# Kernel tuning notes

Hardware: AMD Instinct MI355X
Metric: run time of the kernel (lower is better)

Reference implementation:

```python
import math
import jax, jax.numpy as jnp
import numpy as np

NA = 50000   # number of query nodes
NB = 50000   # number of key/value nodes
E = 800000   # number of edges
CA = 256
CB = 256
D = 256
H = 8
DH = D // H


def setup_inputs() -> dict:
    key = jax.random.key(0)
    ks = jax.random.split(key, 8)
    s = 1.0 / math.sqrt(CA)
    return {
        "Fa": jax.random.normal(ks[0], (NA, CA), dtype=jnp.float32),
        "Fb": jax.random.normal(ks[1], (NB, CB), dtype=jnp.float32),
        "a_idx": jax.random.randint(ks[2], (E,), 0, NA, dtype=jnp.int64)
        if jax.config.jax_enable_x64 else jax.random.randint(ks[2], (E,), 0, NA, dtype=jnp.int32),
        "b_idx": jax.random.randint(ks[3], (E,), 0, NB, dtype=jnp.int64)
        if jax.config.jax_enable_x64 else jax.random.randint(ks[3], (E,), 0, NB, dtype=jnp.int32),
        # torch nn.Linear weights: (out_features, in_features), y = x @ W.T
        "Wq": jax.random.normal(ks[4], (D, CA), dtype=jnp.float32) * s,
        "Wk": jax.random.normal(ks[5], (D, CB), dtype=jnp.float32) * s,
        "Wv": jax.random.normal(ks[6], (D, CB), dtype=jnp.float32) * s,
        "Wproj": jax.random.normal(ks[7], (CA, D), dtype=jnp.float32) * s,
    }


def _edge_attention(Q, K, V, Q_idx, K_idx, n_queries):
    # Q: (Na,H,dh)  K,V: (Nb,H,dh)  Q_idx,K_idx: (E,)
    scale = 1.0 / math.sqrt(Q.shape[-1])
    logits = jnp.sum(Q[Q_idx] * K[K_idx], axis=-1) * scale      # (E, H)
    # segmented softmax over edges sharing the same query (per head)
    seg_max = jax.ops.segment_max(logits, Q_idx, num_segments=n_queries)  # (Na, H)
    seg_max = jnp.where(jnp.isfinite(seg_max), seg_max, 0.0)
    ex = jnp.exp(logits - seg_max[Q_idx])                        # (E, H)
    seg_sum = jax.ops.segment_sum(ex, Q_idx, num_segments=n_queries)      # (Na, H)
    weights = ex / jnp.maximum(seg_sum[Q_idx], 1e-30)            # (E, H)
    # scatter-add weighted values
    out = jax.ops.segment_sum(weights[..., None] * V[K_idx], Q_idx,
                              num_segments=n_queries)            # (Na, H, dh)
    return out


def reference(Fa, Fb, a_idx, b_idx, Wq, Wk, Wv, Wproj):
    Na = Fa.shape[0]
    Q = (Fa @ Wq.T).reshape(Na, H, DH)
    K = (Fb @ Wk.T).reshape(-1, H, DH)
    V = (Fb @ Wv.T).reshape(-1, H, DH)
    out = _edge_attention(Q, K, V, a_idx, b_idx, Na)
    out = out.reshape(Na, H * DH)
    return Fa + out @ Wproj.T
```

## Files before the change

kernel.cpp:

```cpp
#include <hip/hip_runtime.h>

#define DM 256

typedef __attribute__((ext_vector_type(8))) short bf16x8;
typedef __attribute__((ext_vector_type(4))) float f32x4;
typedef __attribute__((ext_vector_type(4))) unsigned short us16x4;
typedef __attribute__((ext_vector_type(8))) unsigned short us16x8;
typedef unsigned short us16;

__device__ __forceinline__ unsigned short f2bf(float f) {
  unsigned int u = __float_as_uint(f);
  u += 0x7fffu + ((u >> 16) & 1u);
  return (unsigned short)(u >> 16);
}
__device__ __forceinline__ float bf2f(unsigned short s) {
  return __uint_as_float(((unsigned int)s) << 16);
}

__device__ __forceinline__ void gload16(const void* g, void* l) {
  __builtin_amdgcn_global_load_lds(
      (const __attribute__((address_space(1))) void*)g,
      (__attribute__((address_space(3))) void*)l, 16, 0, 0);
}

__global__ __launch_bounds__(512) void qkv_gemm(
    const float* __restrict__ Fa, const float* __restrict__ Fb,
    const us16* __restrict__ W_all, us16* __restrict__ Qbf,
    us16* __restrict__ KVbf, int NA, int NB)
{
  const int z = blockIdx.z;
  const float* A = (z == 0) ? Fa : Fb;
  const int Mreal = (z == 0) ? NA : NB;
  const int Mp = (Mreal + 127) & ~127;
  const us16* W = W_all + (size_t)z * 256 * 256;
  us16* Cb = (z == 0) ? Qbf : KVbf;
  const int ldc = (z == 0) ? 256 : 512;

  __shared__ us16 As[128 * 32];
  __shared__ us16 Bs[256 * 32];
  const int tid = threadIdx.x;
  const int w = tid >> 6, l = tid & 63;
  const int wr = w >> 2, wc = w & 3;
  const int rowBase = blockIdx.x * 128;
  if (rowBase >= Mp) return;
  const int ar = tid >> 2, ac = (tid & 3) * 8;
  f32x4 acc[4][4] = {};

  for (int k0 = 0; k0 < 256; k0 += 32) {
#pragma unroll
    for (int j = 0; j < 2; ++j) {
      const int r0 = (w * 2 + j) * 16;
      gload16(W + (size_t)(r0 + (l >> 2)) * 256 + k0 + (l & 3) * 8, &Bs[r0 * 32]);
    }
    {
      const int grow = rowBase + ar;
      bf16x8 av = (bf16x8){0, 0, 0, 0, 0, 0, 0, 0};
      if (grow < Mreal) {
        const float4 x = *(const float4*)(A + (size_t)grow * 256 + k0 + ac);
        const float4 y = *(const float4*)(A + (size_t)grow * 256 + k0 + ac + 4);
        av[0] = (short)f2bf(x.x); av[1] = (short)f2bf(x.y);
        av[2] = (short)f2bf(x.z); av[3] = (short)f2bf(x.w);
        av[4] = (short)f2bf(y.x); av[5] = (short)f2bf(y.y);
        av[6] = (short)f2bf(y.z); av[7] = (short)f2bf(y.w);
      }
      *(bf16x8*)&As[ar * 32 + ac] = av;
    }
    __syncthreads();
    bf16x8 af[4], bfr[4];
#pragma unroll
    for (int m = 0; m < 4; ++m)
      af[m] = *(const bf16x8*)&As[(wr * 64 + m * 16 + (l & 15)) * 32 + (l >> 4) * 8];
#pragma unroll
    for (int n = 0; n < 4; ++n)
      bfr[n] = *(const bf16x8*)&Bs[(wc * 64 + n * 16 + (l & 15)) * 32 + (l >> 4) * 8];
#pragma unroll
    for (int m = 0; m < 4; ++m)
#pragma unroll
      for (int n = 0; n < 4; ++n)
        acc[m][n] = __builtin_amdgcn_mfma_f32_16x16x32_bf16(af[m], bfr[n], acc[m][n], 0, 0, 0);
    __syncthreads();
  }

  const int er = (l >> 4) * 4;
  const int ec = l & 15;
  const int vofs = (z == 2) ? 4 : 0;
#pragma unroll
  for (int m = 0; m < 4; ++m)
#pragma unroll
    for (int n = 0; n < 4; ++n)
#pragma unroll
      for (int j = 0; j < 4; ++j) {
        const int grow = rowBase + wr * 64 + m * 16 + er + j;
        const int c = wc * 64 + n * 16 + ec;
        const int col = (z == 0) ? c : ((c >> 2) * 8 + (c & 3) + vofs);
        Cb[(size_t)grow * ldc + col] = f2bf(acc[m][n][j]);
      }
}

__global__ __launch_bounds__(512) void proj_gemm(
    const us16* __restrict__ A, const us16* __restrict__ W,
    float* __restrict__ Cf, const float* __restrict__ R, int Mreal)
{
  __shared__ us16 As[128 * 32];
  __shared__ us16 Bs[256 * 32];
  const int tid = threadIdx.x;
  const int w = tid >> 6, l = tid & 63;
  const int wr = w >> 2, wc = w & 3;
  const int rowBase = blockIdx.x * 128;
  const int ar = tid >> 2, ac = (tid & 3) * 8;
  f32x4 acc[4][4] = {};

  for (int k0 = 0; k0 < 256; k0 += 32) {
#pragma unroll
    for (int j = 0; j < 2; ++j) {
      const int r0 = (w * 2 + j) * 16;
      gload16(W + (size_t)(r0 + (l >> 2)) * 256 + k0 + (l & 3) * 8, &Bs[r0 * 32]);
    }
    *(bf16x8*)&As[ar * 32 + ac] =
        *(const bf16x8*)(A + (size_t)(rowBase + ar) * 256 + k0 + ac);
    __syncthreads();
    bf16x8 af[4], bfr[4];
#pragma unroll
    for (int m = 0; m < 4; ++m)
      af[m] = *(const bf16x8*)&As[(wr * 64 + m * 16 + (l & 15)) * 32 + (l >> 4) * 8];
#pragma unroll
    for (int n = 0; n < 4; ++n)
      bfr[n] = *(const bf16x8*)&Bs[(wc * 64 + n * 16 + (l & 15)) * 32 + (l >> 4) * 8];
#pragma unroll
    for (int m = 0; m < 4; ++m)
#pragma unroll
      for (int n = 0; n < 4; ++n)
        acc[m][n] = __builtin_amdgcn_mfma_f32_16x16x32_bf16(af[m], bfr[n], acc[m][n], 0, 0, 0);
    __syncthreads();
  }

  const int er = (l >> 4) * 4;
  const int ec = l & 15;
#pragma unroll
  for (int m = 0; m < 4; ++m)
#pragma unroll
    for (int n = 0; n < 4; ++n)
#pragma unroll
      for (int j = 0; j < 4; ++j) {
        const int grow = rowBase + wr * 64 + m * 16 + er + j;
        if (grow < Mreal) {
          const size_t off = (size_t)grow * 256 + wc * 64 + n * 16 + ec;
          Cf[off] = acc[m][n][j] + R[off];
        }
      }
}

__global__ void cvt_weights(const float* __restrict__ Wq, const float* __restrict__ Wk,
                            const float* __restrict__ Wv, const float* __restrict__ Wp,
                            us16* __restrict__ out)
{
  const int g = blockIdx.x * 256 + threadIdx.x;
  const size_t e = (size_t)g * 8;
  const int sel = (int)(e >> 16);
  const float* src = (sel == 0) ? Wq : (sel == 1) ? Wk : (sel == 2) ? Wv : Wp;
  const size_t loc = e & 65535;
  const float4 x = *(const float4*)(src + loc);
  const float4 y = *(const float4*)(src + loc + 4);
  bf16x8 o;
  o[0] = (short)f2bf(x.x); o[1] = (short)f2bf(x.y);
  o[2] = (short)f2bf(x.z); o[3] = (short)f2bf(x.w);
  o[4] = (short)f2bf(y.x); o[5] = (short)f2bf(y.y);
  o[6] = (short)f2bf(y.z); o[7] = (short)f2bf(y.w);
  *(bf16x8*)(out + e) = o;
}

__global__ void hist_kernel(const int* __restrict__ a_idx, int* __restrict__ counts, int E)
{
  const int e = blockIdx.x * 256 + threadIdx.x;
  if (e < E) atomicAdd(&counts[a_idx[e]], 1);
}

__global__ __launch_bounds__(256) void scan_offs(const int* __restrict__ counts,
    int* __restrict__ offs, int* __restrict__ cursor, int* __restrict__ total, int n)
{
  __shared__ int buf[256];
  __shared__ int sbase;
  const int t = threadIdx.x;
  const int i = blockIdx.x * 256 + t;
  const int v = (i < n) ? counts[i] : 0;
  buf[t] = v;
  __syncthreads();
#pragma unroll
  for (int off = 1; off < 256; off <<= 1) {
    const int x = (t >= off) ? buf[t - off] : 0;
    __syncthreads();
    buf[t] += x;
    __syncthreads();
  }
  const int incl = buf[t];
  if (t == 255) sbase = atomicAdd(total, incl);
  __syncthreads();
  if (i < n) {
    const int excl = sbase + incl - v;
    offs[i] = excl;
    cursor[i] = excl;
  }
}

__global__ void scatter_kernel(const int* __restrict__ a_idx, const int* __restrict__ b_idx,
    int* __restrict__ cursor, int* __restrict__ bel, int E)
{
  const int e = blockIdx.x * 256 + threadIdx.x;
  if (e < E) bel[atomicAdd(&cursor[a_idx[e]], 1)] = b_idx[e];
}

#define ATTN_STEP(S, J)                                        \
  if ((J) < cnt) {                                             \
    float p = q0 * bf2f(S[0]);                                 \
    p = fmaf(q1, bf2f(S[1]), p);                               \
    p = fmaf(q2, bf2f(S[2]), p);                               \
    p = fmaf(q3, bf2f(S[3]), p);                               \
    p += __shfl_xor(p, 1, 64);                                 \
    p += __shfl_xor(p, 2, 64);                                 \
    p += __shfl_xor(p, 4, 64);                                 \
    const float ex = __expf(p * scale);                        \
    ssum += ex;                                                \
    acc0 = fmaf(ex, bf2f(S[4]), acc0);                         \
    acc1 = fmaf(ex, bf2f(S[5]), acc1);                         \
    acc2 = fmaf(ex, bf2f(S[6]), acc2);                         \
    acc3 = fmaf(ex, bf2f(S[7]), acc3);                         \
  }

#define ATTN_LOAD(S, IDX)                                      \
  S = *(const us16x8*)(KVb + (size_t)bel[start + (IDX)] * 512 + l * 8);

__global__ __launch_bounds__(256) void edge_attn(
    const us16* __restrict__ Qb, const us16* __restrict__ KVb,
    const int* __restrict__ offs, const int* __restrict__ counts,
    const int* __restrict__ bel, us16* __restrict__ outb, int NA)
{
  const int a = blockIdx.x * 4 + (threadIdx.x >> 6);
  if (a >= NA) return;
  const int l = threadIdx.x & 63;
  const float scale = 0.17677669529663687f;

  const us16x4 q4 = *(const us16x4*)(Qb + (size_t)a * 256 + l * 4);
  const float q0 = bf2f(q4[0]), q1 = bf2f(q4[1]), q2 = bf2f(q4[2]), q3 = bf2f(q4[3]);

  const int start = offs[a];
  const int cnt = counts[a];
  float acc0 = 0.f, acc1 = 0.f, acc2 = 0.f, acc3 = 0.f, ssum = 0.f;

  if (cnt > 0) {
    const int last = cnt - 1;
    us16x8 sa, sb, sc, sd;
    ATTN_LOAD(sa, 0)
    ATTN_LOAD(sb, min(1, last))
    ATTN_LOAD(sc, min(2, last))
    ATTN_LOAD(sd, min(3, last))
    for (int i = 0; i < cnt; i += 4) {
      us16x8 na, nb, nc, nd;
      ATTN_LOAD(na, min(i + 4, last))
      ATTN_LOAD(nb, min(i + 5, last))
      ATTN_LOAD(nc, min(i + 6, last))
      ATTN_LOAD(nd, min(i + 7, last))
      ATTN_STEP(sa, i + 0)
      ATTN_STEP(sb, i + 1)
      ATTN_STEP(sc, i + 2)
      ATTN_STEP(sd, i + 3)
      sa = na; sb = nb; sc = nc; sd = nd;
    }
  }

  const float inv = (cnt > 0) ? 1.f / ssum : 0.f;
  us16x4 o;
  o[0] = f2bf(acc0 * inv); o[1] = f2bf(acc1 * inv);
  o[2] = f2bf(acc2 * inv); o[3] = f2bf(acc3 * inv);
  *(us16x4*)(outb + (size_t)a * 256 + l * 4) = o;
}

extern "C" void kernel_launch(void* const* d_in, const int* in_sizes, int n_in,
                              void* d_out, int out_size, void* d_ws, size_t ws_size,
                              hipStream_t stream)
{
  const float* Fa    = (const float*)d_in[0];
  const float* Fb    = (const float*)d_in[1];
  const int*   a_idx = (const int*)d_in[2];
  const int*   b_idx = (const int*)d_in[3];
  const float* Wq    = (const float*)d_in[4];
  const float* Wk    = (const float*)d_in[5];
  const float* Wv    = (const float*)d_in[6];
  const float* Wproj = (const float*)d_in[7];
  float* out = (float*)d_out;

  const int NA = in_sizes[0] / DM;
  const int NB = in_sizes[1] / DM;
  const int E  = in_sizes[2];
  const int MAp = (NA + 127) & ~127;
  const int NBp = (NB + 127) & ~127;
  const int MXp = (MAp > NBp) ? MAp : NBp;

  us16* Qbf   = (us16*)d_ws;
  us16* KVbf  = Qbf   + (size_t)MAp * 256;
  us16* ATbf  = KVbf  + (size_t)NBp * 512;
  us16* W_all = ATbf  + (size_t)MAp * 256;
  int* total  = (int*)(W_all + 1024 * 256);
  int* counts = total + 1;
  int* offs   = counts + NA;
  int* cursor = offs + NA;
  int* bel    = cursor + NA;

  hipMemsetAsync(total, 0, (size_t)(NA + 1) * sizeof(int), stream);

  cvt_weights<<<128, 256, 0, stream>>>(Wq, Wk, Wv, Wproj, W_all);

  hist_kernel<<<(E + 255) / 256, 256, 0, stream>>>(a_idx, counts, E);
  scan_offs<<<(NA + 255) / 256, 256, 0, stream>>>(counts, offs, cursor, total, NA);
  scatter_kernel<<<(E + 255) / 256, 256, 0, stream>>>(a_idx, b_idx, cursor, bel, E);

  qkv_gemm<<<dim3(MXp / 128, 1, 3), 512, 0, stream>>>(Fa, Fb, W_all, Qbf, KVbf, NA, NB);

  edge_attn<<<(NA + 3) / 4, 256, 0, stream>>>(Qbf, KVbf, offs, counts, bel, ATbf, NA);

  proj_gemm<<<dim3(MAp / 128, 1), 512, 0, stream>>>(ATbf, W_all + 768 * 256, out, Fa, NA);
}
```

Before: 448.3 us.

## Double-buffer LDS tiles in QKV and projection GEMMs to overlap loads with MFMA

Both GEMM kernels now use two LDS buffers for A and B tiles. The next K-slice is prefetched while MFMAs run on the current one, leaving one barrier per iteration instead of two. The projection GEMM also loads its A tile with global_load_lds direct-to-LDS instead of going through registers. This is meant to hide global load latency, at the cost of doubled shared memory (48KB per block), which may limit occupancy.

```diff
diff --git a/kernel.cpp b/kernel.cpp
--- a/kernel.cpp
+++ b/kernel.cpp
@@ -36,48 +36,71 @@
   us16* Cb = (z == 0) ? Qbf : KVbf;
   const int ldc = (z == 0) ? 256 : 512;
 
-  __shared__ us16 As[128 * 32];
-  __shared__ us16 Bs[256 * 32];
+  __shared__ us16 As[2][128 * 32];
+  __shared__ us16 Bs[2][256 * 32];
   const int tid = threadIdx.x;
   const int w = tid >> 6, l = tid & 63;
   const int wr = w >> 2, wc = w & 3;
   const int rowBase = blockIdx.x * 128;
   if (rowBase >= Mp) return;
   const int ar = tid >> 2, ac = (tid & 3) * 8;
+  const int grow0 = rowBase + ar;
+  const bool aval = grow0 < Mreal;
+  const float* Ap = A + (size_t)grow0 * 256 + ac;
   f32x4 acc[4][4] = {};
 
-  for (int k0 = 0; k0 < 256; k0 += 32) {
+  {
+    float4 x = make_float4(0.f, 0.f, 0.f, 0.f), y = x;
+    if (aval) { x = *(const float4*)(Ap); y = *(const float4*)(Ap + 4); }
 #pragma unroll
     for (int j = 0; j < 2; ++j) {
       const int r0 = (w * 2 + j) * 16;
-      gload16(W + (size_t)(r0 + (l >> 2)) * 256 + k0 + (l & 3) * 8, &Bs[r0 * 32]);
-    }
-    {
-      const int grow = rowBase + ar;
-      bf16x8 av = (bf16x8){0, 0, 0, 0, 0, 0, 0, 0};
-      if (grow < Mreal) {
-        const float4 x = *(const float4*)(A + (size_t)grow * 256 + k0 + ac);
-        const float4 y = *(const float4*)(A + (size_t)grow * 256 + k0 + ac + 4);
-        av[0] = (short)f2bf(x.x); av[1] = (short)f2bf(x.y);
-        av[2] = (short)f2bf(x.z); av[3] = (short)f2bf(x.w);
-        av[4] = (short)f2bf(y.x); av[5] = (short)f2bf(y.y);
-        av[6] = (short)f2bf(y.z); av[7] = (short)f2bf(y.w);
+      gload16(W + (size_t)(r0 + (l >> 2)) * 256 + (l & 3) * 8, &Bs[0][r0 * 32]);
+    }
+    bf16x8 av;
+    av[0] = (short)f2bf(x.x); av[1] = (short)f2bf(x.y);
+    av[2] = (short)f2bf(x.z); av[3] = (short)f2bf(x.w);
+    av[4] = (short)f2bf(y.x); av[5] = (short)f2bf(y.y);
+    av[6] = (short)f2bf(y.z); av[7] = (short)f2bf(y.w);
+    *(bf16x8*)&As[0][ar * 32 + ac] = av;
+  }
+  __syncthreads();
+
+  for (int t = 0; t < 8; ++t) {
+    const int cur = t & 1, nxt = cur ^ 1;
+    const bool pf = (t < 7);
+    float4 x, y;
+    if (pf) {
+      const int k0 = (t + 1) * 32;
+      x = make_float4(0.f, 0.f, 0.f, 0.f); y = x;
+      if (aval) { x = *(const float4*)(Ap + k0); y = *(const float4*)(Ap + k0 + 4); }
+#pragma unroll
+      for (int j = 0; j < 2; ++j) {
+        const int r0 = (w * 2 + j) * 16;
+        gload16(W + (size_t)(r0 + (l >> 2)) * 256 + k0 + (l & 3) * 8,
+                &Bs[nxt][r0 * 32]);
       }
-      *(bf16x8*)&As[ar * 32 + ac] = av;
-    }
-    __syncthreads();
+    }
     bf16x8 af[4], bfr[4];
 #pragma unroll
     for (int m = 0; m < 4; ++m)
-      af[m] = *(const bf16x8*)&As[(wr * 64 + m * 16 + (l & 15)) * 32 + (l >> 4) * 8];
+      af[m] = *(const bf16x8*)&As[cur][(wr * 64 + m * 16 + (l & 15)) * 32 + (l >> 4) * 8];
 #pragma unroll
     for (int n = 0; n < 4; ++n)
-      bfr[n] = *(const bf16x8*)&Bs[(wc * 64 + n * 16 + (l & 15)) * 32 + (l >> 4) * 8];
+      bfr[n] = *(const bf16x8*)&Bs[cur][(wc * 64 + n * 16 + (l & 15)) * 32 + (l >> 4) * 8];
 #pragma unroll
     for (int m = 0; m < 4; ++m)
 #pragma unroll
       for (int n = 0; n < 4; ++n)
         acc[m][n] = __builtin_amdgcn_mfma_f32_16x16x32_bf16(af[m], bfr[n], acc[m][n], 0, 0, 0);
+    if (pf) {
+      bf16x8 av;
+      av[0] = (short)f2bf(x.x); av[1] = (short)f2bf(x.y);
+      av[2] = (short)f2bf(x.z); av[3] = (short)f2bf(x.w);
+      av[4] = (short)f2bf(y.x); av[5] = (short)f2bf(y.y);
+      av[6] = (short)f2bf(y.z); av[7] = (short)f2bf(y.w);
+      *(bf16x8*)&As[nxt][ar * 32 + ac] = av;
+    }
     __syncthreads();
   }
 
@@ -101,31 +124,47 @@
     const us16* __restrict__ A, const us16* __restrict__ W,
     float* __restrict__ Cf, const float* __restrict__ R, int Mreal)
 {
-  __shared__ us16 As[128 * 32];
-  __shared__ us16 Bs[256 * 32];
+  __shared__ us16 As[2][128 * 32];
+  __shared__ us16 Bs[2][256 * 32];
   const int tid = threadIdx.x;
   const int w = tid >> 6, l = tid & 63;
   const int wr = w >> 2, wc = w & 3;
   const int rowBase = blockIdx.x * 128;
-  const int ar = tid >> 2, ac = (tid & 3) * 8;
   f32x4 acc[4][4] = {};
 
-  for (int k0 = 0; k0 < 256; k0 += 32) {
+  {
+    const int r0 = w * 16;
+    gload16(A + (size_t)(rowBase + r0 + (l >> 2)) * 256 + (l & 3) * 8,
+            &As[0][r0 * 32]);
 #pragma unroll
     for (int j = 0; j < 2; ++j) {
-      const int r0 = (w * 2 + j) * 16;
-      gload16(W + (size_t)(r0 + (l >> 2)) * 256 + k0 + (l & 3) * 8, &Bs[r0 * 32]);
-    }
-    *(bf16x8*)&As[ar * 32 + ac] =
-        *(const bf16x8*)(A + (size_t)(rowBase + ar) * 256 + k0 + ac);
-    __syncthreads();
+      const int rb = (w * 2 + j) * 16;
+      gload16(W + (size_t)(rb + (l >> 2)) * 256 + (l & 3) * 8, &Bs[0][rb * 32]);
+    }
+  }
+  __syncthreads();
+
+  for (int t = 0; t < 8; ++t) {
+    const int cur = t & 1, nxt = cur ^ 1;
+    if (t < 7) {
+      const int k0 = (t + 1) * 32;
+      const int r0 = w * 16;
+      gload16(A + (size_t)(rowBase + r0 + (l >> 2)) * 256 + k0 + (l & 3) * 8,
+              &As[nxt][r0 * 32]);
+#pragma unroll
+      for (int j = 0; j < 2; ++j) {
+        const int rb = (w * 2 + j) * 16;
+        gload16(W + (size_t)(rb + (l >> 2)) * 256 + k0 + (l & 3) * 8,
+                &Bs[nxt][rb * 32]);
+      }
+    }
     bf16x8 af[4], bfr[4];
 #pragma unroll
     for (int m = 0; m < 4; ++m)
-      af[m] = *(const bf16x8*)&As[(wr * 64 + m * 16 + (l & 15)) * 32 + (l >> 4) * 8];
+      af[m] = *(const bf16x8*)&As[cur][(wr * 64 + m * 16 + (l & 15)) * 32 + (l >> 4) * 8];
 #pragma unroll
     for (int n = 0; n < 4; ++n)
-      bfr[n] = *(const bf16x8*)&Bs[(wc * 64 + n * 16 + (l & 15)) * 32 + (l >> 4) * 8];
+      bfr[n] = *(const bf16x8*)&Bs[cur][(wc * 64 + n * 16 + (l & 15)) * 32 + (l >> 4) * 8];
 #pragma unroll
     for (int m = 0; m < 4; ++m)
 #pragma unroll
```

Result: faster. 438.2 us (-2.3%).
